# Performance work log

Measured on AMD Instinct MI355X. Metric: run time of the kernel, lower is better.

## Reference

```python
import jax, jax.numpy as jnp
import numpy as np
import math

K = 128
H = 8

def setup_inputs() -> dict:
    key = jax.random.key(0)
    ks = jax.random.split(key, 6)
    x = jax.random.normal(ks[0], (4, 2048, K), dtype=jnp.float32)
    # torch nn.Linear weights have shape (out_features, in_features)
    s = 1.0 / math.sqrt(K)
    Wq = jax.random.uniform(ks[1], (K * H, K), minval=-s, maxval=s, dtype=jnp.float32)
    Wk = jax.random.uniform(ks[2], (K * H, K), minval=-s, maxval=s, dtype=jnp.float32)
    Wv = jax.random.uniform(ks[3], (K * H, K), minval=-s, maxval=s, dtype=jnp.float32)
    so = 1.0 / math.sqrt(K * H)
    Wo = jax.random.uniform(ks[4], (K, K * H), minval=-so, maxval=so, dtype=jnp.float32)
    bo = jax.random.uniform(ks[5], (K,), minval=-so, maxval=so, dtype=jnp.float32)
    return {"x": x, "Wq": Wq, "Wk": Wk, "Wv": Wv, "Wo": Wo, "bo": bo}

def reference(x, Wq, Wk, Wv, Wo, bo):
    b, c, k = x.shape
    h = H
    # Linear(k, k*h, bias=False): x @ W.T, then view (b, c, h, k)
    q = (x @ Wq.T).reshape(b, c, h, k)
    kk = (x @ Wk.T).reshape(b, c, h, k)
    v = (x @ Wv.T).reshape(b, c, h, k)
    # Original: einsum('bchk,bihe->bhci') sums k and e INDEPENDENTLY
    # (quirk of the source). Equivalent factored form (same math, cheaper):
    dot = jnp.einsum('bch,bih->bhci', q.sum(-1), kk.sum(-1)) / math.sqrt(k)
    attn = jax.nn.softmax(dot, axis=-1)                      # (b, h, c, c)
    # einsum('bchd,bdce->bhce') on dot(b,h,c,i), values(b,i,h,e):
    out = jnp.einsum('bhti,bihe->bthe', attn, v)             # (b, c, h, k)
    # final: einsum('bthe,khe->btk', out, Wo.view(k, h, k)) + bias
    y = jnp.einsum('bthe,khe->btk', out, Wo.reshape(k, h, k)) + bo
    return y
```

## Files before the change

kernel.cpp:

```cpp
#include <hip/hip_runtime.h>
#include <math.h>

#define NB 4
#define NC 2048
#define NH 8
#define NK 128
#define NG 255

#define A2SCALE (1.4426950408889634f * 0.08838834764831845f)

typedef __attribute__((ext_vector_type(8))) short bf16x8;
typedef __attribute__((ext_vector_type(4))) float f32x4;

#define OFF_W2  8192
#define OFF_MM  8192
#define OFF_QS  139264
#define OFF_KS  204800
#define OFF_U   270336
#define OFF_PN  4464640

__device__ static inline float exp2_hw(float x) {
#if __has_builtin(__builtin_amdgcn_exp2f)
    return __builtin_amdgcn_exp2f(x);
#else
    float r;
    asm volatile("v_exp_f32 %0, %1\n\ts_nop 1" : "=v"(r) : "v"(x));
    return r;
#endif
}

__device__ static inline unsigned cvtpk(float lo, float hi) {
    unsigned r;
    asm("v_cvt_pk_bf16_f32 %0, %1, %2" : "=v"(r) : "v"(lo), "v"(hi));
    return r;
}

__device__ static inline bf16x8 pack8(float4 a, float4 b) {
    union { unsigned u[4]; bf16x8 v; } r;
    r.u[0] = cvtpk(a.x, a.y);
    r.u[1] = cvtpk(a.z, a.w);
    r.u[2] = cvtpk(b.x, b.y);
    r.u[3] = cvtpk(b.z, b.w);
    return r.v;
}

__device__ static inline bf16x8 pexp8s(float4 ka, float4 kb, float a, float negM,
                                       float& z) {
    float e0 = exp2_hw(fmaf(a, ka.x, negM));
    float e1 = exp2_hw(fmaf(a, ka.y, negM));
    float e2 = exp2_hw(fmaf(a, ka.z, negM));
    float e3 = exp2_hw(fmaf(a, ka.w, negM));
    float e4 = exp2_hw(fmaf(a, kb.x, negM));
    float e5 = exp2_hw(fmaf(a, kb.y, negM));
    float e6 = exp2_hw(fmaf(a, kb.z, negM));
    float e7 = exp2_hw(fmaf(a, kb.w, negM));
    z += ((e0 + e1) + (e2 + e3)) + ((e4 + e5) + (e6 + e7));
    union { unsigned u[4]; bf16x8 v; } r;
    r.u[0] = cvtpk(e0, e1);
    r.u[1] = cvtpk(e2, e3);
    r.u[2] = cvtpk(e4, e5);
    r.u[3] = cvtpk(e6, e7);
    return r.v;
}

__global__ __launch_bounds__(256) void k_prep1(const float* __restrict__ Wq,
                                               const float* __restrict__ Wk,
                                               const float* __restrict__ Wv,
                                               const float* __restrict__ Wo,
                                               float* __restrict__ wspart,
                                               float* __restrict__ W2) {
    int blk = blockIdx.x;
    int tid = threadIdx.x;
    __shared__ float sh[256];
    if (blk < 64) {
        int which = blk >> 5, h = (blk >> 2) & 7, eq = blk & 3;
        const float* W = which ? Wk : Wq;
        int m = tid & 127, part = tid >> 7;
        const float* base = W + (h * 128 + eq * 32 + part * 16) * 128 + m;
        float s = 0.f;
#pragma unroll
        for (int e = 0; e < 16; ++e) s += base[e * 128];
        if (part) sh[m] = s;
        __syncthreads();
        if (!part) wspart[eq * 2048 + which * 1024 + h * 128 + m] = s + sh[m];
    } else {
        int idx = blk - 64;
        int h = idx >> 6;
        int kl = tid >> 7;
        int kk = (idx & 63) * 2 + kl;
        int m = tid & 127;
        float* wo_s = sh;
        wo_s[kl * 128 + m] = Wo[kk * 1024 + h * 128 + m];
        __syncthreads();
        const float* base = Wv + (h * 128) * 128 + m;
        const float* wrow = &wo_s[kl * 128];
        float s = 0.f;
#pragma unroll 4
        for (int e = 0; e < 128; ++e) s += base[e * 128] * wrow[e];
        W2[(h * 128 + kk) * 128 + m] = s;
    }
}

__global__ __launch_bounds__(256) void k_prep2(const float* __restrict__ x,
                                               const float* __restrict__ wspart,
                                               const float* __restrict__ W2,
                                               float* __restrict__ qs,
                                               float* __restrict__ ks,
                                               unsigned short* __restrict__ u16) {
    __shared__ __align__(16) unsigned char smem_u8[32768];
    int tid = threadIdx.x;
    int blk = blockIdx.x;
    if (blk < 256) {
        float* xs = (float*)smem_u8;
        float* wsum = (float*)smem_u8 + 32 * 129;
        for (int j = tid; j < 2048; j += 256)
            wsum[j] = wspart[j] + wspart[2048 + j] + wspart[4096 + j] + wspart[6144 + j];
        int row0 = blk * 32;
        for (int j = tid; j < 32 * 128; j += 256) {
            int r = j >> 7, m = j & 127;
            xs[r * 129 + m] = x[(size_t)(row0 + r) * 128 + m];
        }
        __syncthreads();
#pragma unroll
        for (int jj = 0; jj < 2; ++jj) {
            int o = tid + 256 * jj;
            int r = o & 31;
            int q = o >> 5;
            int which = q >> 3, h = q & 7;
            const float* wrow = &wsum[which * 1024 + h * 128];
            const float* xrow = &xs[r * 129];
            float s = 0.f;
#pragma unroll 4
            for (int m = 0; m < 128; ++m) s += xrow[m] * wrow[m];
            int row = row0 + r, b = row >> 11, t = row & 2047;
            float* dst = which ? ks : qs;
            dst[(b * 8 + h) * 2048 + t] = s;
        }
    } else {
        int gid = blk - 256;
        int xcd = gid & 7, s = gid >> 3;
        int bh = xcd * 4 + (s >> 4);
        int it = s & 15;
        int b = bh >> 3, h = bh & 7;
        int lane = tid & 63, wid = tid >> 6;
        int wr = wid >> 1, wc = wid & 1;
        int l15 = lane & 15, l4 = lane >> 4;

        const float* xb = x + (size_t)(b * 2048 + it * 128) * 128;
        const float* w2h = W2 + h * 16384;

        f32x4 acc[4][4];
#pragma unroll
        for (int m = 0; m < 4; ++m)
#pragma unroll
            for (int n = 0; n < 4; ++n) acc[m][n] = (f32x4)0.f;

#pragma unroll
        for (int mg = 0; mg < 4; ++mg) {
            bf16x8 af[4], bfr[4];
#pragma unroll
            for (int m = 0; m < 4; ++m) {
                const float* src = xb + (wr * 64 + m * 16 + l15) * 128 + mg * 32 + l4 * 8;
                af[m] = pack8(*(const float4*)src, *(const float4*)(src + 4));
            }
#pragma unroll
            for (int n = 0; n < 4; ++n) {
                const float* src = w2h + (wc * 64 + n * 16 + l15) * 128 + mg * 32 + l4 * 8;
                bfr[n] = pack8(*(const float4*)src, *(const float4*)(src + 4));
            }
#pragma unroll
            for (int m = 0; m < 4; ++m)
#pragma unroll
                for (int n = 0; n < 4; ++n)
                    acc[m][n] = __builtin_amdgcn_mfma_f32_16x16x32_bf16(
                        af[m], bfr[n], acc[m][n], 0, 0, 0);
        }

        unsigned* u_sh = (unsigned*)smem_u8;
#pragma unroll
        for (int m = 0; m < 4; ++m) {
            int i_base = wr * 64 + m * 16 + l4 * 4;
            int ig = i_base >> 5;
            int lg = 16 * ((i_base >> 3) & 3);
            int jp = (i_base & 7) >> 1;
#pragma unroll
            for (int n = 0; n < 4; ++n) {
                int kk = wc * 64 + n * 16 + l15;
                int lp = (kk & 15) + lg;
                int idx = ((ig * 8 + (kk >> 4)) * 64 + lp) * 4 + jp;
                uint2 w;
                w.x = cvtpk(acc[m][n][0], acc[m][n][1]);
                w.y = cvtpk(acc[m][n][2], acc[m][n][3]);
                *(uint2*)&u_sh[idx] = w;
            }
        }
        __syncthreads();
        unsigned short* ub = u16 + ((size_t)(b * 8 + h) * 64 + it * 4) * 4096;
#pragma unroll
        for (int q = 0; q < 8; ++q)
            ((uint4*)ub)[tid + q * 256] = ((const uint4*)u_sh)[tid + q * 256];
    }
}

__global__ __launch_bounds__(256, 2) void k_table(const float* __restrict__ qs,
                                                  const float* __restrict__ ks,
                                                  const unsigned short* __restrict__ ub,
                                                  float* __restrict__ pN,
                                                  float* __restrict__ pz,
                                                  float* __restrict__ mm) {
    int L = blockIdx.x;
    int xcd = L & 7, s = L >> 3;
    int bh = xcd * 4 + (s >> 4);
    int rem = s & 15;
    int gt = rem >> 2, sl = rem & 3;
    int tid = threadIdx.x;
    int lane = tid & 63, wid = tid >> 6;
    int l15 = lane & 15, l4 = lane >> 4;

    __shared__ float kss[2048];
    __shared__ __align__(16) unsigned short u_l[3][4096];
    __shared__ float red[8];

    for (int j = tid; j < 512; j += 256)
        ((float4*)kss)[j] = ((const float4*)(qs + bh * 2048))[j];
    __syncthreads();
    float mn = 1e30f, mx = -1e30f;
    {
        const float4* ka = (const float4*)kss;
#pragma unroll
        for (int jj = 0; jj < 2; ++jj) {
            float4 v = ka[tid + jj * 256];
            mn = fminf(mn, fminf(fminf(v.x, v.y), fminf(v.z, v.w)));
            mx = fmaxf(mx, fmaxf(fmaxf(v.x, v.y), fmaxf(v.z, v.w)));
        }
#pragma unroll
        for (int off = 32; off; off >>= 1) {
            mn = fminf(mn, __shfl_xor(mn, off));
            mx = fmaxf(mx, __shfl_xor(mx, off));
        }
        if (!lane) { red[wid] = mn; red[4 + wid] = mx; }
    }
    __syncthreads();
    mn = fminf(fminf(red[0], red[1]), fminf(red[2], red[3]));
    mx = fmaxf(fmaxf(red[4], red[5]), fmaxf(red[6], red[7]));
    float amin = mn * A2SCALE;
    float hstep = fmaxf((mx * A2SCALE - amin), 1e-6f) * (1.f / (NG - 1));
    if (tid == 0) { mm[bh * 2] = amin; mm[bh * 2 + 1] = hstep; }
    __syncthreads();

    for (int j = tid; j < 512; j += 256)
        ((float4*)kss)[j] = ((const float4*)(ks + bh * 2048))[j];
    __syncthreads();
    mn = 1e30f; mx = -1e30f;
    {
        const float4* ka = (const float4*)kss;
#pragma unroll
        for (int jj = 0; jj < 2; ++jj) {
            float4 v = ka[tid + jj * 256];
            mn = fminf(mn, fminf(fminf(v.x, v.y), fminf(v.z, v.w)));
            mx = fmaxf(mx, fmaxf(fmaxf(v.x, v.y), fmaxf(v.z, v.w)));
        }
#pragma unroll
        for (int off = 32; off; off >>= 1) {
            mn = fminf(mn, __shfl_xor(mn, off));
            mx = fmaxf(mx, __shfl_xor(mx, off));
        }
        if (!lane) { red[wid] = mn; red[4 + wid] = mx; }
    }
    __syncthreads();
    mn = fminf(fminf(red[0], red[1]), fminf(red[2], red[3]));
    mx = fmaxf(fmaxf(red[4], red[5]), fmaxf(red[6], red[7]));

    int grow = gt * 64 + wid * 16 + l15;
    float a = fmaf((float)grow, hstep, amin);
    float negM = -(a > 0.f ? a * mx : a * mn);
    float zacc = 0.f;

    const unsigned short* gub = ub + (size_t)bh * 262144 + (size_t)sl * 65536;

    f32x4 acc[8];
#pragma unroll
    for (int n = 0; n < 8; ++n) acc[n] = (f32x4)0.f;

#define DMA(cnv, buf) do {                                                     \
    const unsigned short* src_ = gub + (size_t)(cnv) * 4096;                   \
    _Pragma("unroll")                                                          \
    for (int q_ = 0; q_ < 2; ++q_) {                                           \
        int seg_ = q_ * 4 + wid;                                               \
        __builtin_amdgcn_global_load_lds(                                      \
            (const __attribute__((address_space(1))) unsigned int*)(src_ + seg_ * 512 + lane * 8), \
            (__attribute__((address_space(3))) unsigned int*)(&u_l[buf][seg_ * 512]),              \
            16, 0, 0);                                                         \
    }                                                                          \
} while (0)

    DMA(0, 0);
    DMA(1, 1);
    for (int cn = 0; cn < 15; ++cn) {
        int cur = cn % 3;
        int ib = sl * 512 + cn * 32;
        float4 ka = *(const float4*)&kss[ib + l4 * 8];
        float4 kb = *(const float4*)&kss[ib + l4 * 8 + 4];
        bf16x8 pf = pexp8s(ka, kb, a, negM, zacc);

        asm volatile("s_waitcnt vmcnt(2)" ::: "memory");
        __builtin_amdgcn_sched_barrier(0);
        __builtin_amdgcn_s_barrier();
        __builtin_amdgcn_sched_barrier(0);
        if (cn + 2 <= 15) DMA(cn + 2, (cn + 2) % 3);
        __builtin_amdgcn_sched_barrier(0);

        __builtin_amdgcn_s_setprio(1);
#pragma unroll
        for (int n = 0; n < 8; ++n) {
            bf16x8 uf = *(const bf16x8*)&u_l[cur][n * 512 + lane * 8];
            acc[n] = __builtin_amdgcn_mfma_f32_16x16x32_bf16(pf, uf, acc[n], 0, 0, 0);
        }
        __builtin_amdgcn_s_setprio(0);
    }
    {
        int ib = sl * 512 + 15 * 32;
        float4 ka = *(const float4*)&kss[ib + l4 * 8];
        float4 kb = *(const float4*)&kss[ib + l4 * 8 + 4];
        bf16x8 pf = pexp8s(ka, kb, a, negM, zacc);
        asm volatile("s_waitcnt vmcnt(0)" ::: "memory");
        __builtin_amdgcn_sched_barrier(0);
        __builtin_amdgcn_s_barrier();
        __builtin_amdgcn_sched_barrier(0);
#pragma unroll
        for (int n = 0; n < 8; ++n) {
            bf16x8 uf = *(const bf16x8*)&u_l[0][n * 512 + lane * 8];
            acc[n] = __builtin_amdgcn_mfma_f32_16x16x32_bf16(pf, uf, acc[n], 0, 0, 0);
        }
    }
#undef DMA

    zacc += __shfl_xor(zacc, 16);
    zacc += __shfl_xor(zacc, 32);
    if (l4 == 0 && grow < NG)
        pz[(bh * 4 + sl) * NG + grow] = zacc;

#pragma unroll
    for (int r = 0; r < 4; ++r) {
        int g = gt * 64 + wid * 16 + l4 * 4 + r;
        if (g < NG) {
            float* row = pN + ((size_t)(bh * 4 + sl) * NG + g) * 128;
#pragma unroll
            for (int n = 0; n < 8; ++n)
                row[n * 16 + l15] = acc[n][r];
        }
    }
}

__global__ __launch_bounds__(256) void k_reduce(float* __restrict__ pN,
                                                const float* __restrict__ pz) {
    int blk = blockIdx.x;
    int bh = blk >> 3;
    int g = (blk & 7) * 32 + (threadIdx.x >> 3);
    if (g >= NG) return;
    int kq = (threadIdx.x & 7) * 16;
    float z = pz[(bh * 4 + 0) * NG + g] + pz[(bh * 4 + 1) * NG + g] +
              pz[(bh * 4 + 2) * NG + g] + pz[(bh * 4 + 3) * NG + g];
    float zinv = 1.f / z;
    size_t r0 = ((size_t)(bh * 4 + 0) * NG + g) * 128 + kq;
    size_t r1 = ((size_t)(bh * 4 + 1) * NG + g) * 128 + kq;
    size_t r2 = ((size_t)(bh * 4 + 2) * NG + g) * 128 + kq;
    size_t r3 = ((size_t)(bh * 4 + 3) * NG + g) * 128 + kq;
#pragma unroll
    for (int v = 0; v < 4; ++v) {
        float4 s0 = *(const float4*)&pN[r0 + v * 4];
        float4 s1 = *(const float4*)&pN[r1 + v * 4];
        float4 s2 = *(const float4*)&pN[r2 + v * 4];
        float4 s3 = *(const float4*)&pN[r3 + v * 4];
        float4 o;
        o.x = (s0.x + s1.x + s2.x + s3.x) * zinv;
        o.y = (s0.y + s1.y + s2.y + s3.y) * zinv;
        o.z = (s0.z + s1.z + s2.z + s3.z) * zinv;
        o.w = (s0.w + s1.w + s2.w + s3.w) * zinv;
        *(float4*)&pN[r0 + v * 4] = o;
    }
}

__global__ __launch_bounds__(256) void k_eval(const float* __restrict__ qs,
                                              const float* __restrict__ tablef,
                                              const float* __restrict__ mm,
                                              const float* __restrict__ bo,
                                              float* __restrict__ y) {
    int blk = blockIdx.x;
    int b = blk >> 7;
    int t = (blk & 127) * 16 + (threadIdx.x >> 4);
    int kk0 = (threadIdx.x & 15) * 8;

    float acc[8];
#pragma unroll
    for (int j = 0; j < 8; ++j) acc[j] = bo[kk0 + j];

#pragma unroll
    for (int h = 0; h < 8; ++h) {
        int bh = b * 8 + h;
        float a = qs[bh * 2048 + t] * A2SCALE;
        float amin = mm[bh * 2], hs = mm[bh * 2 + 1];
        float p = (a - amin) / hs;
        int g1 = (int)p;
        g1 = g1 < 1 ? 1 : (g1 > NG - 3 ? NG - 3 : g1);
        float u = p - (float)g1;
        float um1 = u - 1.f, um2 = u - 2.f, up1 = u + 1.f;
        float w0 = -u * um1 * um2 * (1.f / 6.f);
        float w1 = up1 * um1 * um2 * 0.5f;
        float w2 = -up1 * u * um2 * 0.5f;
        float w3 = up1 * u * um1 * (1.f / 6.f);
        const float* base = tablef + ((size_t)(bh * 4) * NG + (g1 - 1)) * 128 + kk0;
#pragma unroll
        for (int v = 0; v < 2; ++v) {
            float4 r0 = *(const float4*)(base + v * 4);
            float4 r1 = *(const float4*)(base + 128 + v * 4);
            float4 r2 = *(const float4*)(base + 256 + v * 4);
            float4 r3 = *(const float4*)(base + 384 + v * 4);
            acc[v * 4 + 0] += w0 * r0.x + w1 * r1.x + w2 * r2.x + w3 * r3.x;
            acc[v * 4 + 1] += w0 * r0.y + w1 * r1.y + w2 * r2.y + w3 * r3.y;
            acc[v * 4 + 2] += w0 * r0.z + w1 * r1.z + w2 * r2.z + w3 * r3.z;
            acc[v * 4 + 3] += w0 * r0.w + w1 * r1.w + w2 * r2.w + w3 * r3.w;
        }
    }
    float* yp = y + ((size_t)b * 2048 + t) * 128 + kk0;
    *(float4*)yp = make_float4(acc[0], acc[1], acc[2], acc[3]);
    *(float4*)(yp + 4) = make_float4(acc[4], acc[5], acc[6], acc[7]);
}

extern "C" void kernel_launch(void* const* d_in, const int* in_sizes, int n_in,
                              void* d_out, int out_size, void* d_ws, size_t ws_size,
                              hipStream_t stream) {
    const float* x  = (const float*)d_in[0];
    const float* Wq = (const float*)d_in[1];
    const float* Wk = (const float*)d_in[2];
    const float* Wv = (const float*)d_in[3];
    const float* Wo = (const float*)d_in[4];
    const float* bo = (const float*)d_in[5];
    float* y  = (float*)d_out;
    float* ws = (float*)d_ws;
    (void)in_sizes; (void)n_in; (void)out_size; (void)ws_size;

    unsigned short* u16 = (unsigned short*)(ws + OFF_U);
    float* pN = ws + OFF_PN;
    float* pz = y;
    float* mm = ws + OFF_MM;

    k_prep1<<<576, 256, 0, stream>>>(Wq, Wk, Wv, Wo, ws, ws + OFF_W2);
    k_prep2<<<768, 256, 0, stream>>>(x, ws, ws + OFF_W2, ws + OFF_QS, ws + OFF_KS, u16);
    k_table<<<512, 256, 0, stream>>>(ws + OFF_QS, ws + OFF_KS, u16, pN, pz, mm);
    k_reduce<<<256, 256, 0, stream>>>(pN, pz);
    k_eval<<<512, 256, 0, stream>>>(ws + OFF_QS, pN, mm, bo, y);
}
```

Before: 65.14 us.

## Reassociate value projection: contract attention table with bf16 x, apply W2 afterwards

Instead of precomputing a per-head bf16 projected-value tensor x·W2 for every batch and head, prep2 now writes only a bf16 copy of x in MFMA-friendly layout. The table kernel contracts the softmax weights with that copy, which is shared across the 8 heads of a batch. A new kernel then sums the split partials, multiplies by W2 with MFMA and normalises by z, replacing the separate reduce kernel. This removes the large U tensor write and read plus its GEMM, at the cost of an extra small GEMM on the grouped table. It also moves the mm buffer onto the now-dead workspace region.

```diff
diff --git a/kernel.cpp b/kernel.cpp
--- a/kernel.cpp
+++ b/kernel.cpp
@@ -12,11 +12,11 @@
 typedef __attribute__((ext_vector_type(8))) short bf16x8;
 typedef __attribute__((ext_vector_type(4))) float f32x4;
 
+#define OFF_MM  0
 #define OFF_W2  8192
-#define OFF_MM  8192
 #define OFF_QS  139264
 #define OFF_KS  204800
-#define OFF_U   270336
+#define OFF_XB  270336
 #define OFF_PN  4464640
 
 __device__ static inline float exp2_hw(float x) {
@@ -103,116 +103,68 @@
 
 __global__ __launch_bounds__(256) void k_prep2(const float* __restrict__ x,
                                                const float* __restrict__ wspart,
-                                               const float* __restrict__ W2,
                                                float* __restrict__ qs,
                                                float* __restrict__ ks,
-                                               unsigned short* __restrict__ u16) {
-    __shared__ __align__(16) unsigned char smem_u8[32768];
+                                               unsigned short* __restrict__ xbf) {
+    __shared__ float xs[32][129];
+    __shared__ float wsum[2048];
     int tid = threadIdx.x;
     int blk = blockIdx.x;
-    if (blk < 256) {
-        float* xs = (float*)smem_u8;
-        float* wsum = (float*)smem_u8 + 32 * 129;
-        for (int j = tid; j < 2048; j += 256)
-            wsum[j] = wspart[j] + wspart[2048 + j] + wspart[4096 + j] + wspart[6144 + j];
-        int row0 = blk * 32;
-        for (int j = tid; j < 32 * 128; j += 256) {
-            int r = j >> 7, m = j & 127;
-            xs[r * 129 + m] = x[(size_t)(row0 + r) * 128 + m];
-        }
-        __syncthreads();
-#pragma unroll
-        for (int jj = 0; jj < 2; ++jj) {
-            int o = tid + 256 * jj;
-            int r = o & 31;
-            int q = o >> 5;
-            int which = q >> 3, h = q & 7;
-            const float* wrow = &wsum[which * 1024 + h * 128];
-            const float* xrow = &xs[r * 129];
-            float s = 0.f;
+    for (int j = tid; j < 2048; j += 256)
+        wsum[j] = wspart[j] + wspart[2048 + j] + wspart[4096 + j] + wspart[6144 + j];
+    int row0 = blk * 32;
+    for (int j = tid; j < 32 * 128; j += 256) {
+        int r = j >> 7, m = j & 127;
+        xs[r][m] = x[(size_t)(row0 + r) * 128 + m];
+    }
+    __syncthreads();
+#pragma unroll
+    for (int jj = 0; jj < 2; ++jj) {
+        int o = tid + 256 * jj;
+        int r = o & 31;
+        int q = o >> 5;
+        int which = q >> 3, h = q & 7;
+        const float* wrow = &wsum[which * 1024 + h * 128];
+        const float* xrow = &xs[r][0];
+        float s = 0.f;
 #pragma unroll 4
-            for (int m = 0; m < 128; ++m) s += xrow[m] * wrow[m];
-            int row = row0 + r, b = row >> 11, t = row & 2047;
-            float* dst = which ? ks : qs;
-            dst[(b * 8 + h) * 2048 + t] = s;
-        }
-    } else {
-        int gid = blk - 256;
-        int xcd = gid & 7, s = gid >> 3;
-        int bh = xcd * 4 + (s >> 4);
-        int it = s & 15;
-        int b = bh >> 3, h = bh & 7;
-        int lane = tid & 63, wid = tid >> 6;
-        int wr = wid >> 1, wc = wid & 1;
-        int l15 = lane & 15, l4 = lane >> 4;
-
-        const float* xb = x + (size_t)(b * 2048 + it * 128) * 128;
-        const float* w2h = W2 + h * 16384;
-
-        f32x4 acc[4][4];
-#pragma unroll
-        for (int m = 0; m < 4; ++m)
-#pragma unroll
-            for (int n = 0; n < 4; ++n) acc[m][n] = (f32x4)0.f;
-
-#pragma unroll
-        for (int mg = 0; mg < 4; ++mg) {
-            bf16x8 af[4], bfr[4];
-#pragma unroll
-            for (int m = 0; m < 4; ++m) {
-                const float* src = xb + (wr * 64 + m * 16 + l15) * 128 + mg * 32 + l4 * 8;
-                af[m] = pack8(*(const float4*)src, *(const float4*)(src + 4));
-            }
-#pragma unroll
-            for (int n = 0; n < 4; ++n) {
-                const float* src = w2h + (wc * 64 + n * 16 + l15) * 128 + mg * 32 + l4 * 8;
-                bfr[n] = pack8(*(const float4*)src, *(const float4*)(src + 4));
-            }
-#pragma unroll
-            for (int m = 0; m < 4; ++m)
-#pragma unroll
-                for (int n = 0; n < 4; ++n)
-                    acc[m][n] = __builtin_amdgcn_mfma_f32_16x16x32_bf16(
-                        af[m], bfr[n], acc[m][n], 0, 0, 0);
-        }
-
-        unsigned* u_sh = (unsigned*)smem_u8;
-#pragma unroll
-        for (int m = 0; m < 4; ++m) {
-            int i_base = wr * 64 + m * 16 + l4 * 4;
-            int ig = i_base >> 5;
-            int lg = 16 * ((i_base >> 3) & 3);
-            int jp = (i_base & 7) >> 1;
-#pragma unroll
-            for (int n = 0; n < 4; ++n) {
-                int kk = wc * 64 + n * 16 + l15;
-                int lp = (kk & 15) + lg;
-                int idx = ((ig * 8 + (kk >> 4)) * 64 + lp) * 4 + jp;
-                uint2 w;
-                w.x = cvtpk(acc[m][n][0], acc[m][n][1]);
-                w.y = cvtpk(acc[m][n][2], acc[m][n][3]);
-                *(uint2*)&u_sh[idx] = w;
-            }
-        }
-        __syncthreads();
-        unsigned short* ub = u16 + ((size_t)(b * 8 + h) * 64 + it * 4) * 4096;
-#pragma unroll
-        for (int q = 0; q < 8; ++q)
-            ((uint4*)ub)[tid + q * 256] = ((const uint4*)u_sh)[tid + q * 256];
-    }
-}
-
-__global__ __launch_bounds__(256, 2) void k_table(const float* __restrict__ qs,
-                                                  const float* __restrict__ ks,
-                                                  const unsigned short* __restrict__ ub,
-                                                  float* __restrict__ pN,
-                                                  float* __restrict__ pz,
-                                                  float* __restrict__ mm) {
+        for (int m = 0; m < 128; ++m) s += xrow[m] * wrow[m];
+        int row = row0 + r, b = row >> 11, t = row & 2047;
+        float* dst = which ? ks : qs;
+        dst[(b * 8 + h) * 2048 + t] = s;
+    }
+    {
+        int b = row0 >> 11;
+        int ig = (row0 >> 5) & 63;
+        unsigned short* xb = xbf + (size_t)(b * 64 + ig) * 4096;
+#pragma unroll
+        for (int qq = 0; qq < 2; ++qq) {
+            int q = tid + qq * 256;
+            int nt = q >> 6, lane = q & 63;
+            int l4 = lane >> 4, m = nt * 16 + (lane & 15);
+            int ib = l4 * 8;
+            union { unsigned u[4]; uint4 v; } pk;
+            pk.u[0] = cvtpk(xs[ib + 0][m], xs[ib + 1][m]);
+            pk.u[1] = cvtpk(xs[ib + 2][m], xs[ib + 3][m]);
+            pk.u[2] = cvtpk(xs[ib + 4][m], xs[ib + 5][m]);
+            pk.u[3] = cvtpk(xs[ib + 6][m], xs[ib + 7][m]);
+            *(uint4*)&xb[(size_t)nt * 512 + lane * 8] = pk.v;
+        }
+    }
+}
+
+__global__ __launch_bounds__(256, 2) void k_c(const float* __restrict__ qs,
+                                              const float* __restrict__ ks,
+                                              const unsigned short* __restrict__ xbf,
+                                              float* __restrict__ pC,
+                                              float* __restrict__ pz,
+                                              float* __restrict__ mm) {
     int L = blockIdx.x;
     int xcd = L & 7, s = L >> 3;
     int bh = xcd * 4 + (s >> 4);
     int rem = s & 15;
     int gt = rem >> 2, sl = rem & 3;
+    int b = bh >> 3;
     int tid = threadIdx.x;
     int lane = tid & 63, wid = tid >> 6;
     int l15 = lane & 15, l4 = lane >> 4;
@@ -276,14 +228,14 @@
     float negM = -(a > 0.f ? a * mx : a * mn);
     float zacc = 0.f;
 
-    const unsigned short* gub = ub + (size_t)bh * 262144 + (size_t)sl * 65536;
+    const unsigned short* gxb = xbf + (size_t)b * 262144 + (size_t)sl * 65536;
 
     f32x4 acc[8];
 #pragma unroll
     for (int n = 0; n < 8; ++n) acc[n] = (f32x4)0.f;
 
 #define DMA(cnv, buf) do {                                                     \
-    const unsigned short* src_ = gub + (size_t)(cnv) * 4096;                   \
+    const unsigned short* src_ = gxb + (size_t)(cnv) * 4096;                   \
     _Pragma("unroll")                                                          \
     for (int q_ = 0; q_ < 2; ++q_) {                                           \
         int seg_ = q_ * 4 + wid;                                               \
@@ -344,7 +296,7 @@
     for (int r = 0; r < 4; ++r) {
         int g = gt * 64 + wid * 16 + l4 * 4 + r;
         if (g < NG) {
-            float* row = pN + ((size_t)(bh * 4 + sl) * NG + g) * 128;
+            float* row = pC + ((size_t)(bh * 4 + sl) * NG + g) * 128;
 #pragma unroll
             for (int n = 0; n < 8; ++n)
                 row[n * 16 + l15] = acc[n][r];
@@ -352,32 +304,76 @@
     }
 }
 
-__global__ __launch_bounds__(256) void k_reduce(float* __restrict__ pN,
-                                                const float* __restrict__ pz) {
-    int blk = blockIdx.x;
-    int bh = blk >> 3;
-    int g = (blk & 7) * 32 + (threadIdx.x >> 3);
-    if (g >= NG) return;
-    int kq = (threadIdx.x & 7) * 16;
-    float z = pz[(bh * 4 + 0) * NG + g] + pz[(bh * 4 + 1) * NG + g] +
-              pz[(bh * 4 + 2) * NG + g] + pz[(bh * 4 + 3) * NG + g];
-    float zinv = 1.f / z;
-    size_t r0 = ((size_t)(bh * 4 + 0) * NG + g) * 128 + kq;
-    size_t r1 = ((size_t)(bh * 4 + 1) * NG + g) * 128 + kq;
-    size_t r2 = ((size_t)(bh * 4 + 2) * NG + g) * 128 + kq;
-    size_t r3 = ((size_t)(bh * 4 + 3) * NG + g) * 128 + kq;
-#pragma unroll
-    for (int v = 0; v < 4; ++v) {
-        float4 s0 = *(const float4*)&pN[r0 + v * 4];
-        float4 s1 = *(const float4*)&pN[r1 + v * 4];
-        float4 s2 = *(const float4*)&pN[r2 + v * 4];
-        float4 s3 = *(const float4*)&pN[r3 + v * 4];
-        float4 o;
-        o.x = (s0.x + s1.x + s2.x + s3.x) * zinv;
-        o.y = (s0.y + s1.y + s2.y + s3.y) * zinv;
-        o.z = (s0.z + s1.z + s2.z + s3.z) * zinv;
-        o.w = (s0.w + s1.w + s2.w + s3.w) * zinv;
-        *(float4*)&pN[r0 + v * 4] = o;
+__global__ __launch_bounds__(256) void k_n(float* __restrict__ pC,
+                                           const float* __restrict__ pz,
+                                           const float* __restrict__ W2) {
+    int L = blockIdx.x;
+    int bh = L >> 2, gt = L & 3;
+    int h = bh & 7;
+    int tid = threadIdx.x;
+    int lane = tid & 63, wid = tid >> 6;
+    int wr = wid >> 1, wc = wid & 1;
+    int l15 = lane & 15, l4 = lane >> 4;
+
+    const float* w2h = W2 + h * 16384;
+    const size_t slo = (size_t)NG * 128;
+    const size_t cb = (size_t)(bh * 4) * NG * 128;
+
+    f32x4 acc[2][4];
+#pragma unroll
+    for (int mg = 0; mg < 2; ++mg)
+#pragma unroll
+        for (int nt = 0; nt < 4; ++nt) acc[mg][nt] = (f32x4)0.f;
+
+#pragma unroll
+    for (int kq = 0; kq < 4; ++kq) {
+        bf16x8 af[2], bfr[4];
+#pragma unroll
+        for (int mg = 0; mg < 2; ++mg) {
+            int g = gt * 64 + wr * 32 + mg * 16 + l15;
+            size_t base = cb + (size_t)g * 128 + kq * 32 + l4 * 8;
+            float4 sa = *(const float4*)&pC[base];
+            float4 sb = *(const float4*)&pC[base + 4];
+#pragma unroll
+            for (int sl = 1; sl < 4; ++sl) {
+                float4 ta = *(const float4*)&pC[base + sl * slo];
+                float4 tb = *(const float4*)&pC[base + sl * slo + 4];
+                sa.x += ta.x; sa.y += ta.y; sa.z += ta.z; sa.w += ta.w;
+                sb.x += tb.x; sb.y += tb.y; sb.z += tb.z; sb.w += tb.w;
+            }
+            af[mg] = pack8(sa, sb);
+        }
+#pragma unroll
+        for (int nt = 0; nt < 4; ++nt) {
+            int kk = wc * 64 + nt * 16 + l15;
+            const float* src = w2h + kk * 128 + kq * 32 + l4 * 8;
+            bfr[nt] = pack8(*(const float4*)src, *(const float4*)(src + 4));
+        }
+#pragma unroll
+        for (int mg = 0; mg < 2; ++mg)
+#pragma unroll
+            for (int nt = 0; nt < 4; ++nt)
+                acc[mg][nt] = __builtin_amdgcn_mfma_f32_16x16x32_bf16(
+                    af[mg], bfr[nt], acc[mg][nt], 0, 0, 0);
+    }
+
+    __syncthreads();
+
+#pragma unroll
+    for (int mg = 0; mg < 2; ++mg) {
+#pragma unroll
+        for (int r = 0; r < 4; ++r) {
+            int g = gt * 64 + wr * 32 + mg * 16 + l4 * 4 + r;
+            if (g < NG) {
+                float z = pz[(bh * 4 + 0) * NG + g] + pz[(bh * 4 + 1) * NG + g] +
+                          pz[(bh * 4 + 2) * NG + g] + pz[(bh * 4 + 3) * NG + g];
+                float zinv = 1.f / z;
+                float* row = pC + cb + (size_t)g * 128;
+#pragma unroll
+                for (int nt = 0; nt < 4; ++nt)
+                    row[wc * 64 + nt * 16 + l15] = acc[mg][nt][r] * zinv;
+            }
+        }
     }
 }
 
@@ -440,14 +436,14 @@
     float* ws = (float*)d_ws;
     (void)in_sizes; (void)n_in; (void)out_size; (void)ws_size;
 
-    unsigned short* u16 = (unsigned short*)(ws + OFF_U);
-    float* pN = ws + OFF_PN;
+    unsigned short* xbf = (unsigned short*)(ws + OFF_XB);
+    float* pC = ws + OFF_PN;
     float* pz = y;
     float* mm = ws + OFF_MM;
 
     k_prep1<<<576, 256, 0, stream>>>(Wq, Wk, Wv, Wo, ws, ws + OFF_W2);
-    k_prep2<<<768, 256, 0, stream>>>(x, ws, ws + OFF_W2, ws + OFF_QS, ws + OFF_KS, u16);
-    k_table<<<512, 256, 0, stream>>>(ws + OFF_QS, ws + OFF_KS, u16, pN, pz, mm);
-    k_reduce<<<256, 256, 0, stream>>>(pN, pz);
-    k_eval<<<512, 256, 0, stream>>>(ws + OFF_QS, pN, mm, bo, y);
-}
+    k_prep2<<<256, 256, 0, stream>>>(x, ws, ws + OFF_QS, ws + OFF_KS, xbf);
+    k_c<<<512, 256, 0, stream>>>(ws + OFF_QS, ws + OFF_KS, xbf, pC, pz, mm);
+    k_n<<<128, 256, 0, stream>>>(pC, pz, ws + OFF_W2);
+    k_eval<<<512, 256, 0, stream>>>(ws + OFF_QS, pC, mm, bo, y);
+}
```

Result: slower. 68.13 us (+4.6%).

## Compute per-head q/k min-max in prep2 via atomics, drop table-kernel reductions

Applied to the files above, without the earlier changes.

Moves the per-(batch,head) min/max of q-sums and k-sums out of k_table into k_prep2. There each 32-row group reduces with shuffles and issues order-preserving encoded atomicMin/atomicMax, after k_prep1 initialises the slots. k_table then reads four scalars and loads only its own 512-element slice of ks into shared memory, instead of loading and reducing both full 2048-element arrays with several barriers. This removes redundant reductions repeated across 16 blocks per head and cuts LDS use, at the cost of global atomics in prep2 and recomputing hstep in k_eval.

```diff
diff --git a/kernel.cpp b/kernel.cpp
--- a/kernel.cpp
+++ b/kernel.cpp
@@ -12,12 +12,12 @@
 typedef __attribute__((ext_vector_type(8))) short bf16x8;
 typedef __attribute__((ext_vector_type(4))) float f32x4;
 
-#define OFF_W2  8192
-#define OFF_MM  8192
-#define OFF_QS  139264
-#define OFF_KS  204800
-#define OFF_U   270336
-#define OFF_PN  4464640
+#define OFF_W2   8192
+#define OFF_QS   139264
+#define OFF_KS   204800
+#define OFF_U    270336
+#define OFF_PN   4464640
+#define OFF_MMU  8642560
 
 __device__ static inline float exp2_hw(float x) {
 #if __has_builtin(__builtin_amdgcn_exp2f)
@@ -42,6 +42,14 @@
     r.u[2] = cvtpk(b.x, b.y);
     r.u[3] = cvtpk(b.z, b.w);
     return r.v;
+}
+
+__device__ static inline unsigned fenc(float f) {
+    unsigned b = __float_as_uint(f);
+    return (b & 0x80000000u) ? ~b : (b | 0x80000000u);
+}
+__device__ static inline float fdec(unsigned k) {
+    return __uint_as_float((k & 0x80000000u) ? (k & 0x7FFFFFFFu) : ~k);
 }
 
 __device__ static inline bf16x8 pexp8s(float4 ka, float4 kb, float a, float negM,
@@ -68,7 +76,8 @@
                                                const float* __restrict__ Wv,
                                                const float* __restrict__ Wo,
                                                float* __restrict__ wspart,
-                                               float* __restrict__ W2) {
+                                               float* __restrict__ W2,
+                                               unsigned* __restrict__ mmu) {
     int blk = blockIdx.x;
     int tid = threadIdx.x;
     __shared__ float sh[256];
@@ -83,6 +92,8 @@
         if (part) sh[m] = s;
         __syncthreads();
         if (!part) wspart[eq * 2048 + which * 1024 + h * 128 + m] = s + sh[m];
+        if (blk == 0 && tid < 128)
+            mmu[tid] = (tid & 1) ? 0u : 0xFFFFFFFFu;
     } else {
         int idx = blk - 64;
         int h = idx >> 6;
@@ -106,7 +117,8 @@
                                                const float* __restrict__ W2,
                                                float* __restrict__ qs,
                                                float* __restrict__ ks,
-                                               unsigned short* __restrict__ u16) {
+                                               unsigned short* __restrict__ u16,
+                                               unsigned* __restrict__ mmu) {
     __shared__ __align__(16) unsigned char smem_u8[32768];
     int tid = threadIdx.x;
     int blk = blockIdx.x;
@@ -135,6 +147,17 @@
             int row = row0 + r, b = row >> 11, t = row & 2047;
             float* dst = which ? ks : qs;
             dst[(b * 8 + h) * 2048 + t] = s;
+            float gmn = s, gmx = s;
+#pragma unroll
+            for (int off = 1; off <= 16; off <<= 1) {
+                gmn = fminf(gmn, __shfl_xor(gmn, off));
+                gmx = fmaxf(gmx, __shfl_xor(gmx, off));
+            }
+            if (r == 0) {
+                unsigned* mb = &mmu[(b * 8 + h) * 4 + which * 2];
+                atomicMin(&mb[0], fenc(gmn));
+                atomicMax(&mb[1], fenc(gmx));
+            }
         }
     } else {
         int gid = blk - 256;
@@ -202,12 +225,11 @@
     }
 }
 
-__global__ __launch_bounds__(256, 2) void k_table(const float* __restrict__ qs,
-                                                  const float* __restrict__ ks,
+__global__ __launch_bounds__(256, 2) void k_table(const float* __restrict__ ks,
                                                   const unsigned short* __restrict__ ub,
+                                                  const unsigned* __restrict__ mmu,
                                                   float* __restrict__ pN,
-                                                  float* __restrict__ pz,
-                                                  float* __restrict__ mm) {
+                                                  float* __restrict__ pz) {
     int L = blockIdx.x;
     int xcd = L & 7, s = L >> 3;
     int bh = xcd * 4 + (s >> 4);
@@ -217,63 +239,21 @@
     int lane = tid & 63, wid = tid >> 6;
     int l15 = lane & 15, l4 = lane >> 4;
 
-    __shared__ float kss[2048];
+    __shared__ float ks_s[512];
     __shared__ __align__(16) unsigned short u_l[3][4096];
-    __shared__ float red[8];
-
-    for (int j = tid; j < 512; j += 256)
-        ((float4*)kss)[j] = ((const float4*)(qs + bh * 2048))[j];
-    __syncthreads();
-    float mn = 1e30f, mx = -1e30f;
-    {
-        const float4* ka = (const float4*)kss;
-#pragma unroll
-        for (int jj = 0; jj < 2; ++jj) {
-            float4 v = ka[tid + jj * 256];
-            mn = fminf(mn, fminf(fminf(v.x, v.y), fminf(v.z, v.w)));
-            mx = fmaxf(mx, fmaxf(fmaxf(v.x, v.y), fmaxf(v.z, v.w)));
-        }
-#pragma unroll
-        for (int off = 32; off; off >>= 1) {
-            mn = fminf(mn, __shfl_xor(mn, off));
-            mx = fmaxf(mx, __shfl_xor(mx, off));
-        }
-        if (!lane) { red[wid] = mn; red[4 + wid] = mx; }
-    }
-    __syncthreads();
-    mn = fminf(fminf(red[0], red[1]), fminf(red[2], red[3]));
-    mx = fmaxf(fmaxf(red[4], red[5]), fmaxf(red[6], red[7]));
-    float amin = mn * A2SCALE;
-    float hstep = fmaxf((mx * A2SCALE - amin), 1e-6f) * (1.f / (NG - 1));
-    if (tid == 0) { mm[bh * 2] = amin; mm[bh * 2 + 1] = hstep; }
-    __syncthreads();
-
-    for (int j = tid; j < 512; j += 256)
-        ((float4*)kss)[j] = ((const float4*)(ks + bh * 2048))[j];
-    __syncthreads();
-    mn = 1e30f; mx = -1e30f;
-    {
-        const float4* ka = (const float4*)kss;
-#pragma unroll
-        for (int jj = 0; jj < 2; ++jj) {
-            float4 v = ka[tid + jj * 256];
-            mn = fminf(mn, fminf(fminf(v.x, v.y), fminf(v.z, v.w)));
-            mx = fmaxf(mx, fmaxf(fmaxf(v.x, v.y), fmaxf(v.z, v.w)));
-        }
-#pragma unroll
-        for (int off = 32; off; off >>= 1) {
-            mn = fminf(mn, __shfl_xor(mn, off));
-            mx = fmaxf(mx, __shfl_xor(mx, off));
-        }
-        if (!lane) { red[wid] = mn; red[4 + wid] = mx; }
-    }
-    __syncthreads();
-    mn = fminf(fminf(red[0], red[1]), fminf(red[2], red[3]));
-    mx = fmaxf(fmaxf(red[4], red[5]), fmaxf(red[6], red[7]));
+
+    float amin = fdec(mmu[bh * 4]) * A2SCALE;
+    float amax = fdec(mmu[bh * 4 + 1]) * A2SCALE;
+    float hstep = fmaxf(amax - amin, 1e-6f) * (1.f / (NG - 1));
+    float kmn = fdec(mmu[bh * 4 + 2]);
+    float kmx = fdec(mmu[bh * 4 + 3]);
+
+    if (tid < 128)
+        ((float4*)ks_s)[tid] = ((const float4*)(ks + bh * 2048 + sl * 512))[tid];
 
     int grow = gt * 64 + wid * 16 + l15;
     float a = fmaf((float)grow, hstep, amin);
-    float negM = -(a > 0.f ? a * mx : a * mn);
+    float negM = -(a > 0.f ? a * kmx : a * kmn);
     float zacc = 0.f;
 
     const unsigned short* gub = ub + (size_t)bh * 262144 + (size_t)sl * 65536;
@@ -281,6 +261,8 @@
     f32x4 acc[8];
 #pragma unroll
     for (int n = 0; n < 8; ++n) acc[n] = (f32x4)0.f;
+
+    __syncthreads();
 
 #define DMA(cnv, buf) do {                                                     \
     const unsigned short* src_ = gub + (size_t)(cnv) * 4096;                   \
@@ -298,9 +280,8 @@
     DMA(1, 1);
     for (int cn = 0; cn < 15; ++cn) {
         int cur = cn % 3;
-        int ib = sl * 512 + cn * 32;
-        float4 ka = *(const float4*)&kss[ib + l4 * 8];
-        float4 kb = *(const float4*)&kss[ib + l4 * 8 + 4];
+        float4 ka = *(const float4*)&ks_s[cn * 32 + l4 * 8];
+        float4 kb = *(const float4*)&ks_s[cn * 32 + l4 * 8 + 4];
         bf16x8 pf = pexp8s(ka, kb, a, negM, zacc);
 
         asm volatile("s_waitcnt vmcnt(2)" ::: "memory");
@@ -319,9 +300,8 @@
         __builtin_amdgcn_s_setprio(0);
     }
     {
-        int ib = sl * 512 + 15 * 32;
-        float4 ka = *(const float4*)&kss[ib + l4 * 8];
-        float4 kb = *(const float4*)&kss[ib + l4 * 8 + 4];
+        float4 ka = *(const float4*)&ks_s[15 * 32 + l4 * 8];
+        float4 kb = *(const float4*)&ks_s[15 * 32 + l4 * 8 + 4];
         bf16x8 pf = pexp8s(ka, kb, a, negM, zacc);
         asm volatile("s_waitcnt vmcnt(0)" ::: "memory");
         __builtin_amdgcn_sched_barrier(0);
@@ -383,7 +363,7 @@
 
 __global__ __launch_bounds__(256) void k_eval(const float* __restrict__ qs,
                                               const float* __restrict__ tablef,
-                                              const float* __restrict__ mm,
+                                              const unsigned* __restrict__ mmu,
                                               const float* __restrict__ bo,
                                               float* __restrict__ y) {
     int blk = blockIdx.x;
@@ -399,7 +379,9 @@
     for (int h = 0; h < 8; ++h) {
         int bh = b * 8 + h;
         float a = qs[bh * 2048 + t] * A2SCALE;
-        float amin = mm[bh * 2], hs = mm[bh * 2 + 1];
+        float amin = fdec(mmu[bh * 4]) * A2SCALE;
+        float amax = fdec(mmu[bh * 4 + 1]) * A2SCALE;
+        float hs = fmaxf(amax - amin, 1e-6f) * (1.f / (NG - 1));
         float p = (a - amin) / hs;
         int g1 = (int)p;
         g1 = g1 < 1 ? 1 : (g1 > NG - 3 ? NG - 3 : g1);
@@ -441,13 +423,14 @@
     (void)in_sizes; (void)n_in; (void)out_size; (void)ws_size;
 
     unsigned short* u16 = (unsigned short*)(ws + OFF_U);
+    unsigned* mmu = (unsigned*)(ws + OFF_MMU);
     float* pN = ws + OFF_PN;
     float* pz = y;
-    float* mm = ws + OFF_MM;
-
-    k_prep1<<<576, 256, 0, stream>>>(Wq, Wk, Wv, Wo, ws, ws + OFF_W2);
-    k_prep2<<<768, 256, 0, stream>>>(x, ws, ws + OFF_W2, ws + OFF_QS, ws + OFF_KS, u16);
-    k_table<<<512, 256, 0, stream>>>(ws + OFF_QS, ws + OFF_KS, u16, pN, pz, mm);
+
+    k_prep1<<<576, 256, 0, stream>>>(Wq, Wk, Wv, Wo, ws, ws + OFF_W2, mmu);
+    k_prep2<<<768, 256, 0, stream>>>(x, ws, ws + OFF_W2, ws + OFF_QS, ws + OFF_KS,
+                                     u16, mmu);
+    k_table<<<512, 256, 0, stream>>>(ws + OFF_KS, u16, mmu, pN, pz);
     k_reduce<<<256, 256, 0, stream>>>(pN, pz);
-    k_eval<<<512, 256, 0, stream>>>(ws + OFF_QS, pN, mm, bo, y);
-}
+    k_eval<<<512, 256, 0, stream>>>(ws + OFF_QS, pN, mmu, bo, y);
+}
```

Result: slower. 71.95 us (+10.5%).

## Fuse split-K reduction into table kernel via last-block atomic counter

Applied to the files above, without the earlier changes.

Removes the separate k_reduce launch. Each k_table block bumps an atomic counter for its (bh, gt) tile, and the last of the four slice blocks to arrive sums the partial numerators and normalizers and writes the normalized rows in place. The counters are zeroed in k_prep1. This saves one kernel launch and its tail gap, at the cost of threadfences, an atomic per block, and a serialized reduction tail done by only some blocks.

```diff
diff --git a/kernel.cpp b/kernel.cpp
--- a/kernel.cpp
+++ b/kernel.cpp
@@ -12,12 +12,13 @@
 typedef __attribute__((ext_vector_type(8))) short bf16x8;
 typedef __attribute__((ext_vector_type(4))) float f32x4;
 
-#define OFF_W2  8192
-#define OFF_MM  8192
-#define OFF_QS  139264
-#define OFF_KS  204800
-#define OFF_U   270336
-#define OFF_PN  4464640
+#define OFF_W2   8192
+#define OFF_MM   8192
+#define OFF_QS   139264
+#define OFF_KS   204800
+#define OFF_U    270336
+#define OFF_PN   4464640
+#define OFF_CNT  8642560
 
 __device__ static inline float exp2_hw(float x) {
 #if __has_builtin(__builtin_amdgcn_exp2f)
@@ -68,7 +69,8 @@
                                                const float* __restrict__ Wv,
                                                const float* __restrict__ Wo,
                                                float* __restrict__ wspart,
-                                               float* __restrict__ W2) {
+                                               float* __restrict__ W2,
+                                               unsigned* __restrict__ cnt) {
     int blk = blockIdx.x;
     int tid = threadIdx.x;
     __shared__ float sh[256];
@@ -83,6 +85,7 @@
         if (part) sh[m] = s;
         __syncthreads();
         if (!part) wspart[eq * 2048 + which * 1024 + h * 128 + m] = s + sh[m];
+        if (blk == 0 && tid < 128) cnt[tid] = 0u;
     } else {
         int idx = blk - 64;
         int h = idx >> 6;
@@ -207,7 +210,8 @@
                                                   const unsigned short* __restrict__ ub,
                                                   float* __restrict__ pN,
                                                   float* __restrict__ pz,
-                                                  float* __restrict__ mm) {
+                                                  float* __restrict__ mm,
+                                                  unsigned* __restrict__ cnt) {
     int L = blockIdx.x;
     int xcd = L & 7, s = L >> 3;
     int bh = xcd * 4 + (s >> 4);
@@ -220,6 +224,7 @@
     __shared__ float kss[2048];
     __shared__ __align__(16) unsigned short u_l[3][4096];
     __shared__ float red[8];
+    __shared__ unsigned oldc;
 
     for (int j = tid; j < 512; j += 256)
         ((float4*)kss)[j] = ((const float4*)(qs + bh * 2048))[j];
@@ -350,34 +355,32 @@
                 row[n * 16 + l15] = acc[n][r];
         }
     }
-}
-
-__global__ __launch_bounds__(256) void k_reduce(float* __restrict__ pN,
-                                                const float* __restrict__ pz) {
-    int blk = blockIdx.x;
-    int bh = blk >> 3;
-    int g = (blk & 7) * 32 + (threadIdx.x >> 3);
-    if (g >= NG) return;
-    int kq = (threadIdx.x & 7) * 16;
-    float z = pz[(bh * 4 + 0) * NG + g] + pz[(bh * 4 + 1) * NG + g] +
-              pz[(bh * 4 + 2) * NG + g] + pz[(bh * 4 + 3) * NG + g];
-    float zinv = 1.f / z;
-    size_t r0 = ((size_t)(bh * 4 + 0) * NG + g) * 128 + kq;
-    size_t r1 = ((size_t)(bh * 4 + 1) * NG + g) * 128 + kq;
-    size_t r2 = ((size_t)(bh * 4 + 2) * NG + g) * 128 + kq;
-    size_t r3 = ((size_t)(bh * 4 + 3) * NG + g) * 128 + kq;
-#pragma unroll
-    for (int v = 0; v < 4; ++v) {
-        float4 s0 = *(const float4*)&pN[r0 + v * 4];
-        float4 s1 = *(const float4*)&pN[r1 + v * 4];
-        float4 s2 = *(const float4*)&pN[r2 + v * 4];
-        float4 s3 = *(const float4*)&pN[r3 + v * 4];
-        float4 o;
-        o.x = (s0.x + s1.x + s2.x + s3.x) * zinv;
-        o.y = (s0.y + s1.y + s2.y + s3.y) * zinv;
-        o.z = (s0.z + s1.z + s2.z + s3.z) * zinv;
-        o.w = (s0.w + s1.w + s2.w + s3.w) * zinv;
-        *(float4*)&pN[r0 + v * 4] = o;
+
+    __threadfence();
+    if (tid == 0) oldc = atomicAdd(&cnt[bh * 4 + gt], 1u);
+    __syncthreads();
+    if (oldc == 3u) {
+        __threadfence();
+        const size_t slo = (size_t)NG * 128;
+        int g = gt * 64 + (tid >> 2);
+        if (g < NG) {
+            float z = pz[(bh * 4 + 0) * NG + g] + pz[(bh * 4 + 1) * NG + g] +
+                      pz[(bh * 4 + 2) * NG + g] + pz[(bh * 4 + 3) * NG + g];
+            float zinv = 1.f / z;
+            size_t r0 = ((size_t)(bh * 4) * NG + g) * 128;
+            for (int v = (tid & 3); v < 32; v += 4) {
+                float4 s0 = *(const float4*)&pN[r0 + v * 4];
+                float4 s1 = *(const float4*)&pN[r0 + slo + v * 4];
+                float4 s2 = *(const float4*)&pN[r0 + 2 * slo + v * 4];
+                float4 s3 = *(const float4*)&pN[r0 + 3 * slo + v * 4];
+                float4 o;
+                o.x = (s0.x + s1.x + s2.x + s3.x) * zinv;
+                o.y = (s0.y + s1.y + s2.y + s3.y) * zinv;
+                o.z = (s0.z + s1.z + s2.z + s3.z) * zinv;
+                o.w = (s0.w + s1.w + s2.w + s3.w) * zinv;
+                *(float4*)&pN[r0 + v * 4] = o;
+            }
+        }
     }
 }
 
@@ -441,13 +444,13 @@
     (void)in_sizes; (void)n_in; (void)out_size; (void)ws_size;
 
     unsigned short* u16 = (unsigned short*)(ws + OFF_U);
+    unsigned* cnt = (unsigned*)(ws + OFF_CNT);
     float* pN = ws + OFF_PN;
     float* pz = y;
     float* mm = ws + OFF_MM;
 
-    k_prep1<<<576, 256, 0, stream>>>(Wq, Wk, Wv, Wo, ws, ws + OFF_W2);
+    k_prep1<<<576, 256, 0, stream>>>(Wq, Wk, Wv, Wo, ws, ws + OFF_W2, cnt);
     k_prep2<<<768, 256, 0, stream>>>(x, ws, ws + OFF_W2, ws + OFF_QS, ws + OFF_KS, u16);
-    k_table<<<512, 256, 0, stream>>>(ws + OFF_QS, ws + OFF_KS, u16, pN, pz, mm);
-    k_reduce<<<256, 256, 0, stream>>>(pN, pz);
+    k_table<<<512, 256, 0, stream>>>(ws + OFF_QS, ws + OFF_KS, u16, pN, pz, mm, cnt);
     k_eval<<<512, 256, 0, stream>>>(ws + OFF_QS, pN, mm, bo, y);
 }
```

Result: slower. 139.1 us (+113.5%).
